# Performance work log

Measured on AMD Instinct MI355X. Metric: run time of the kernel, lower is better.

The kernel has to match this reference:

```python
import jax, jax.numpy as jnp
import numpy as np

NUM_HEADS = 16
HIDDEN = 1024
HEAD_DIM = HIDDEN // NUM_HEADS
B, S, D = 2, 2048, 1024


def setup_inputs() -> dict:
    key = jax.random.key(0)
    ks = jax.random.split(key, 7)
    scale = 1.0 / np.sqrt(D)
    return {
        "query": jax.random.normal(ks[0], (B, S, D), dtype=jnp.float32),
        "key": jax.random.normal(ks[1], (B, S, D), dtype=jnp.float32),
        "value": jax.random.normal(ks[2], (B, S, D), dtype=jnp.float32),
        "Wk_w": jax.random.normal(ks[3], (HIDDEN, D), dtype=jnp.float32) * scale,
        "Wk_b": jax.random.normal(ks[4], (HIDDEN,), dtype=jnp.float32) * scale,
        "Wv_w": jax.random.normal(ks[5], (HIDDEN, D), dtype=jnp.float32) * scale,
        "Wv_b": jax.random.normal(ks[6], (HIDDEN,), dtype=jnp.float32) * scale,
    }


def reference(query, key, value, Wk_w, Wk_b, Wv_w, Wv_b):
    # NOTE: in the original torch module, self.W_v is assigned twice, so the
    # SAME Linear (Wv) projects both key and value; Wk projects query.
    b, s, _ = query.shape

    def split_heads(x):  # [b,s,hidden] -> [b,h,s,hd]
        return x.reshape(b, s, NUM_HEADS, HEAD_DIM).transpose(0, 2, 1, 3)

    q = split_heads(query @ Wk_w.T + Wk_b)
    k = split_heads(key @ Wv_w.T + Wv_b)
    v = split_heads(value @ Wv_w.T + Wv_b)

    scores = jnp.einsum("bhqd,bhkd->bhqk", q, k) / jnp.sqrt(
        jnp.asarray(HEAD_DIM, dtype=q.dtype))
    probs = jax.nn.softmax(scores, axis=-1)
    out = jnp.einsum("bhqk,bhkd->bhqd", probs, v)
    return out.transpose(0, 2, 1, 3).reshape(b, s, NUM_HEADS * HEAD_DIM)
```

## Files before the change

### kernel.cpp

```cpp
#include <hip/hip_runtime.h>
#include <stdint.h>

typedef unsigned short u16;
typedef uint32_t u32;
typedef __bf16 bf16x8 __attribute__((ext_vector_type(8)));
typedef float f32x4 __attribute__((ext_vector_type(4)));
typedef float f32x16 __attribute__((ext_vector_type(16)));
typedef u16 u16x4 __attribute__((ext_vector_type(4)));
typedef u16 u16x8 __attribute__((ext_vector_type(8)));

#define XQ_OFF 0ul
#define XK_OFF 4194304ul
#define XV_OFF 8388608ul
#define WK_OFF 12582912ul
#define WV_OFF 13631488ul
#define Q_OFF  14680064ul
#define K_OFF  18874368ul
#define V_OFF  23068672ul

#define SCQ 0.18033688011112042f

#if __has_builtin(__builtin_amdgcn_exp2f)
#define EXP2F(x) __builtin_amdgcn_exp2f(x)
#else
#define EXP2F(x) exp2f(x)
#endif

__device__ __forceinline__ u16 f2bf(float f) {
  u32 u = __float_as_uint(f);
  u32 r = (u + 0x7fffu + ((u >> 16) & 1u)) >> 16;
  return (u16)r;
}

__device__ __forceinline__ u32 pk2(float a, float b) {
  typedef __bf16 bf2_t __attribute__((ext_vector_type(2)));
  typedef float f2_t __attribute__((ext_vector_type(2)));
  f2_t v; v[0] = a; v[1] = b;
  bf2_t h = __builtin_convertvector(v, bf2_t);
  union { bf2_t h; u32 u; } cv; cv.h = h; return cv.u;
}

__device__ __forceinline__ void load_lds16(const void* g, void* l) {
  __builtin_amdgcn_global_load_lds(
      (const __attribute__((address_space(1))) u32*)g,
      (__attribute__((address_space(3))) u32*)l, 16, 0, 0);
}

__global__ __launch_bounds__(256) void cvt_tile_kernel(
    const float* __restrict__ xq, const float* __restrict__ xk,
    const float* __restrict__ xv, const float* __restrict__ wk,
    const float* __restrict__ wv, u16* __restrict__ ws) {
  __shared__ u16 tile[4096];
  const int bid = blockIdx.x;
  const float* src; size_t dstbase; int rt, ktp;
  if (bid < 3072) {
    int m = bid >> 10, loc = bid & 1023;
    src = (m == 0) ? xq : (m == 1) ? xk : xv;
    dstbase = (size_t)m * 4194304ul;
    rt = loc >> 4; ktp = loc & 15;
  } else {
    int r2 = bid - 3072;
    int m = r2 >> 8, loc = r2 & 255;
    src = m ? wv : wk;
    dstbase = WK_OFF + (size_t)m * 1048576ul;
    rt = loc >> 4; ktp = loc & 15;
  }
  const int t = threadIdx.x;
  const int row0 = t >> 4, c = t & 15;
  const int k = c * 4;
  const float* s = src + (size_t)(rt * 64 + row0) * 1024ul + ktp * 64 + k;
#pragma unroll
  for (int i = 0; i < 4; ++i) {
    float4 v = *(const float4*)(s + (size_t)i * 16384ul);
    int row = row0 + i * 16;
    u32* p = (u32*)(tile + ((k >> 5) * 2048 + ((k >> 3) & 3) * 512 + row * 8 + (k & 7)));
    p[0] = pk2(v.x, v.y);
    p[1] = pk2(v.z, v.w);
  }
  __syncthreads();
  u16* dst = ws + dstbase + (size_t)(rt * 32 + ktp * 2) * 2048ul;
#pragma unroll
  for (int so = 0; so < 4096; so += 2048)
    *(u16x8*)(dst + so + t * 8) = *(const u16x8*)(tile + so + t * 8);
}

__global__ __launch_bounds__(256, 3) void proj_kernel(u16* __restrict__ ws,
                                                      const float* __restrict__ bk,
                                                      const float* __restrict__ bv) {
  const int proj = blockIdx.z;
  const int mtile = blockIdx.x;
  const int ntile = blockIdx.y;
  const u16* A = ws + (size_t)proj * 4194304ul;
  const u16* Bw = ws + ((proj == 0) ? WK_OFF : WV_OFF);
  const float* bias = (proj == 0) ? bk : bv;
  u16* outQ = ws + Q_OFF;
  u16* outK = ws + K_OFF;
  u16* outV = ws + V_OFF;

  const int t = threadIdx.x;
  const int w = t >> 6, lane = t & 63;
  const int wm = w >> 1, wn = w & 1;
  const int c32 = lane & 31, g2 = lane >> 5;

  const u16* Aw = A + (size_t)(2 * mtile + wm) * 65536ul + (size_t)g2 * 512ul + (size_t)c32 * 8ul;
  const u16* Bb = Bw + (size_t)(2 * ntile + wn) * 65536ul + (size_t)g2 * 512ul + (size_t)c32 * 8ul;

  f32x16 acc[2][2];
#pragma unroll
  for (int rf = 0; rf < 2; ++rf)
#pragma unroll
    for (int cf = 0; cf < 2; ++cf)
#pragma unroll
      for (int i = 0; i < 16; ++i) acc[rf][cf][i] = 0.f;

  bf16x8 ab[4][2], bb[4][2];
#pragma unroll
  for (int s = 0; s < 4; ++s)
#pragma unroll
    for (int f = 0; f < 2; ++f) {
      ab[s][f] = *(const bf16x8*)(Aw + (size_t)s * 1024ul + f * 256);
      bb[s][f] = *(const bf16x8*)(Bb + (size_t)s * 1024ul + f * 256);
    }

#pragma unroll 1
  for (int ks = 0; ks < 60; ks += 4) {
#pragma unroll
    for (int s = 0; s < 4; ++s) {
#pragma unroll
      for (int rf = 0; rf < 2; ++rf)
#pragma unroll
        for (int cf = 0; cf < 2; ++cf)
          acc[rf][cf] =
              __builtin_amdgcn_mfma_f32_32x32x16_bf16(ab[s][rf], bb[s][cf], acc[rf][cf], 0, 0, 0);
      const size_t o = (size_t)(ks + 4 + s) * 1024ul;
#pragma unroll
      for (int f = 0; f < 2; ++f) {
        ab[s][f] = *(const bf16x8*)(Aw + o + f * 256);
        bb[s][f] = *(const bf16x8*)(Bb + o + f * 256);
      }
    }
  }
#pragma unroll
  for (int s = 0; s < 4; ++s)
#pragma unroll
    for (int rf = 0; rf < 2; ++rf)
#pragma unroll
      for (int cf = 0; cf < 2; ++cf)
        acc[rf][cf] =
            __builtin_amdgcn_mfma_f32_32x32x16_bf16(ab[s][rf], bb[s][cf], acc[rf][cf], 0, 0, 0);

  const int m0w = mtile * 128 + wm * 64, n0w = ntile * 128 + wn * 64;
#pragma unroll
  for (int cf = 0; cf < 2; ++cf) {
    const int col = n0w + cf * 32 + c32;
    const float bvv = bias[col];
    const int h = col >> 6, d = col & 63;
#pragma unroll
    for (int rf = 0; rf < 2; ++rf) {
#pragma unroll
      for (int q = 0; q < 4; ++q) {
        const int mbase = m0w + rf * 32 + q * 8 + g2 * 4;
        const int b = mbase >> 11;
        const int bh = b * 16 + h;
        if (proj == 2) {
          const int s = mbase & 2047;
          u16x4 pk;
#pragma unroll
          for (int r = 0; r < 4; ++r) pk[r] = f2bf(acc[rf][cf][q * 4 + r] + bvv);
          size_t idx = (size_t)bh * 131072ul + (size_t)(s >> 6) * 4096ul +
                       (size_t)((s & 63) >> 3) * 512ul + (size_t)d * 8ul + (size_t)(s & 7);
          *(u16x4*)(outV + idx) = pk;
        } else {
          u16* dst = (proj == 0) ? outQ : outK;
#pragma unroll
          for (int r = 0; r < 4; ++r) {
            const int m = mbase + r;
            const int s = m & 2047;
            float y = acc[rf][cf][q * 4 + r] + bvv;
            if (proj == 0) y *= SCQ;
            size_t idx;
            if (proj == 0)
              idx = (size_t)bh * 131072ul + (size_t)(s >> 7) * 8192ul + (size_t)(d >> 3) * 1024ul +
                    (size_t)(s & 127) * 8ul + (size_t)(d & 7);
            else
              idx = (size_t)bh * 131072ul + (size_t)(s >> 6) * 4096ul + (size_t)(d >> 3) * 512ul +
                    (size_t)(s & 63) * 8ul + (size_t)(d & 7);
            dst[idx] = f2bf(y);
          }
        }
      }
    }
  }
}

__global__ __launch_bounds__(256, 2) void attn_kernel(const u16* __restrict__ ws,
                                                      float* __restrict__ out) {
  const int bh = blockIdx.x, qtile = blockIdx.y;
  const int b = bh >> 4, h = bh & 15;
  const int t = threadIdx.x, w = t >> 6, lane = t & 63, g = lane >> 4, c = lane & 15;

  __shared__ __align__(16) u16 Ps[4][1280];

  const u16* Qg = ws + Q_OFF + (size_t)bh * 131072ul + (size_t)qtile * 8192ul;
  const u16* Kg = ws + K_OFF + (size_t)bh * 131072ul;
  const u16* Vg = ws + V_OFF + (size_t)bh * 131072ul;

  bf16x8 qf[2][2];
#pragma unroll
  for (int ntq = 0; ntq < 2; ++ntq)
#pragma unroll
    for (int ks = 0; ks < 2; ++ks)
      qf[ntq][ks] = *(const bf16x8*)(Qg + (ks * 4 + g) * 1024 + (w * 32 + ntq * 16 + c) * 8);

  u16x8 ou;
#pragma unroll
  for (int i = 0; i < 8; ++i) ou[i] = (u16)0x3F80;
  union { u16x8 u; bf16x8 b; } ocv; ocv.u = ou;
  const bf16x8 onesf = ocv.b;

  f32x4 O[2][4], Lacc[2];
#pragma unroll
  for (int mtq = 0; mtq < 2; ++mtq) {
    Lacc[mtq] = (f32x4){0.f, 0.f, 0.f, 0.f};
#pragma unroll
    for (int nt = 0; nt < 4; ++nt) O[mtq][nt] = (f32x4){0.f, 0.f, 0.f, 0.f};
  }

  u16* Psw = Ps[w];

  bf16x8 kf[2][4];
#pragma unroll
  for (int ks = 0; ks < 2; ++ks)
#pragma unroll
    for (int mtk = 0; mtk < 4; ++mtk)
      kf[ks][mtk] = *(const bf16x8*)(Kg + (ks * 4 + g) * 512 + (mtk * 16 + c) * 8);

#pragma unroll 1
  for (int j = 0; j < 32; ++j) {
    const u16* Vj = Vg + (size_t)j * 4096ul;
    bf16x8 vf[2][4];
#pragma unroll
    for (int ksh = 0; ksh < 2; ++ksh)
#pragma unroll
      for (int nt = 0; nt < 4; ++nt)
        vf[ksh][nt] = *(const bf16x8*)(Vj + (ksh * 4 + g) * 512 + (nt * 16 + c) * 8);

    f32x4 St[4][2];
#pragma unroll
    for (int mtk = 0; mtk < 4; ++mtk)
#pragma unroll
      for (int ntq = 0; ntq < 2; ++ntq) St[mtk][ntq] = (f32x4){0.f, 0.f, 0.f, 0.f};
#pragma unroll
    for (int ks = 0; ks < 2; ++ks)
#pragma unroll
      for (int mtk = 0; mtk < 4; ++mtk)
#pragma unroll
        for (int ntq = 0; ntq < 2; ++ntq)
          St[mtk][ntq] =
              __builtin_amdgcn_mfma_f32_16x16x32_bf16(kf[ks][mtk], qf[ntq][ks], St[mtk][ntq], 0, 0, 0);

    const u16* Kn = Kg + (size_t)((j < 31) ? (j + 1) : 31) * 4096ul;
#pragma unroll
    for (int ks = 0; ks < 2; ++ks)
#pragma unroll
      for (int mtk = 0; mtk < 4; ++mtk)
        kf[ks][mtk] = *(const bf16x8*)(Kn + (ks * 4 + g) * 512 + (mtk * 16 + c) * 8);

#pragma unroll
    for (int mtk = 0; mtk < 4; ++mtk)
#pragma unroll
      for (int ntq = 0; ntq < 2; ++ntq)
#pragma unroll
        for (int r = 0; r < 4; ++r) St[mtk][ntq][r] = EXP2F(St[mtk][ntq][r]);

#pragma unroll
    for (int ksh = 0; ksh < 2; ++ksh) {
#pragma unroll
      for (int ntq = 0; ntq < 2; ++ntq)
#pragma unroll
        for (int m2 = 0; m2 < 2; ++m2) {
          const int mtk = ksh * 2 + m2;
          u32 lo = pk2(St[mtk][ntq][0], St[mtk][ntq][1]);
          u32 hi = pk2(St[mtk][ntq][2], St[mtk][ntq][3]);
          u32* p = (u32*)(Psw + (ntq * 16 + c) * 40 + m2 * 16 + g * 4);
          p[0] = lo; p[1] = hi;
        }
      asm volatile("s_waitcnt lgkmcnt(0)" ::: "memory");
      bf16x8 pf[2];
#pragma unroll
      for (int mtq = 0; mtq < 2; ++mtq)
        pf[mtq] = *(const bf16x8*)(Psw + (mtq * 16 + c) * 40 + g * 8);
#pragma unroll
      for (int mtq = 0; mtq < 2; ++mtq) {
        Lacc[mtq] = __builtin_amdgcn_mfma_f32_16x16x32_bf16(pf[mtq], onesf, Lacc[mtq], 0, 0, 0);
#pragma unroll
        for (int nt = 0; nt < 4; ++nt)
          O[mtq][nt] =
              __builtin_amdgcn_mfma_f32_16x16x32_bf16(pf[mtq], vf[ksh][nt], O[mtq][nt], 0, 0, 0);
      }
    }
  }

  const int q0 = qtile * 128 + w * 32;
#pragma unroll
  for (int mtq = 0; mtq < 2; ++mtq)
#pragma unroll
    for (int r = 0; r < 4; ++r) {
      const float inv = 1.0f / Lacc[mtq][r];
      const int q = q0 + mtq * 16 + g * 4 + r;
      float* rowp = out + (size_t)(b * 2048 + q) * 1024ul + h * 64;
#pragma unroll
      for (int nt = 0; nt < 4; ++nt) rowp[nt * 16 + c] = O[mtq][nt][r] * inv;
    }
}

extern "C" void kernel_launch(void* const* d_in, const int* in_sizes, int n_in,
                              void* d_out, int out_size, void* d_ws, size_t ws_size,
                              hipStream_t stream) {
  const float* q = (const float*)d_in[0];
  const float* k = (const float*)d_in[1];
  const float* v = (const float*)d_in[2];
  const float* wk = (const float*)d_in[3];
  const float* bk = (const float*)d_in[4];
  const float* wv = (const float*)d_in[5];
  const float* bv = (const float*)d_in[6];
  u16* ws = (u16*)d_ws;
  float* out = (float*)d_out;

  cvt_tile_kernel<<<3584, 256, 0, stream>>>(q, k, v, wk, wv, ws);
  proj_kernel<<<dim3(32, 8, 3), 256, 0, stream>>>(ws, bk, bv);
  attn_kernel<<<dim3(32, 16), 256, 0, stream>>>(ws, out);
}
```

Before: 180.0 us.

## Stage projection and K/V tiles through swizzled double-buffered LDS

The projection GEMM now loads A and B tiles into double-buffered LDS with direct global-to-LDS copies and an XOR swizzle, computing with 16x16x32 MFMAs instead of per-wave register streaming from global memory. The attention kernel likewise shares each K/V block across all four waves through double-buffered swizzled LDS rather than each wave reading its own copy. It also halves the query rows per block and doubles the grid, with higher occupancy bounds. This is meant to cut redundant global/L2 traffic and raise parallelism, at the cost of a block-wide barrier every iteration and more LDS use.

```diff
diff --git a/kernel.cpp b/kernel.cpp
--- a/kernel.cpp
+++ b/kernel.cpp
@@ -5,7 +5,6 @@
 typedef uint32_t u32;
 typedef __bf16 bf16x8 __attribute__((ext_vector_type(8)));
 typedef float f32x4 __attribute__((ext_vector_type(4)));
-typedef float f32x16 __attribute__((ext_vector_type(16)));
 typedef u16 u16x4 __attribute__((ext_vector_type(4)));
 typedef u16 u16x8 __attribute__((ext_vector_type(8)));
 
@@ -44,6 +43,10 @@
   __builtin_amdgcn_global_load_lds(
       (const __attribute__((address_space(1))) u32*)g,
       (__attribute__((address_space(3))) u32*)l, 16, 0, 0);
+}
+
+__device__ __forceinline__ u32 swz(u32 L) {
+  return L ^ (((L >> 7) & 1u) << 4) ^ (((L >> 10) & 3u) << 5);
 }
 
 __global__ __launch_bounds__(256) void cvt_tile_kernel(
@@ -100,117 +103,131 @@
   const int t = threadIdx.x;
   const int w = t >> 6, lane = t & 63;
   const int wm = w >> 1, wn = w & 1;
-  const int c32 = lane & 31, g2 = lane >> 5;
-
-  const u16* Aw = A + (size_t)(2 * mtile + wm) * 65536ul + (size_t)g2 * 512ul + (size_t)c32 * 8ul;
-  const u16* Bb = Bw + (size_t)(2 * ntile + wn) * 65536ul + (size_t)g2 * 512ul + (size_t)c32 * 8ul;
-
-  f32x16 acc[2][2];
-#pragma unroll
-  for (int rf = 0; rf < 2; ++rf)
-#pragma unroll
-    for (int cf = 0; cf < 2; ++cf)
-#pragma unroll
-      for (int i = 0; i < 16; ++i) acc[rf][cf][i] = 0.f;
-
-  bf16x8 ab[4][2], bb[4][2];
-#pragma unroll
-  for (int s = 0; s < 4; ++s)
-#pragma unroll
-    for (int f = 0; f < 2; ++f) {
-      ab[s][f] = *(const bf16x8*)(Aw + (size_t)s * 1024ul + f * 256);
-      bb[s][f] = *(const bf16x8*)(Bb + (size_t)s * 1024ul + f * 256);
-    }
+  const int g = lane >> 4, c = lane & 15;
+
+  __shared__ __align__(16) u16 As[2][2][2048];
+  __shared__ __align__(16) u16 Bs[2][2][2048];
+
+  const u16* Ag = A + (size_t)(2 * mtile) * 65536ul;
+  const u16* Bg = Bw + (size_t)(2 * ntile) * 65536ul;
+  const u32 t8 = (u32)t * 8u;
+  const u32 so = swz((u32)t * 16u) >> 1;
+
+  u32 poff[4];
+#pragma unroll
+  for (int mt = 0; mt < 4; ++mt)
+    poff[mt] = swz((u32)((g << 10) | ((mt * 16 + c) << 4))) >> 1;
+
+#define PSTAGE(buf, kt)                                            \
+  do {                                                             \
+    const size_t ko = (size_t)(kt) * 2048ul + so;                  \
+    load_lds16(Ag + ko, &As[buf][0][t8]);                          \
+    load_lds16(Ag + 65536ul + ko, &As[buf][1][t8]);                \
+    load_lds16(Bg + ko, &Bs[buf][0][t8]);                          \
+    load_lds16(Bg + 65536ul + ko, &Bs[buf][1][t8]);                \
+  } while (0)
+
+  f32x4 acc[4][4];
+#pragma unroll
+  for (int mt = 0; mt < 4; ++mt)
+#pragma unroll
+    for (int nt = 0; nt < 4; ++nt) acc[mt][nt] = (f32x4){0.f, 0.f, 0.f, 0.f};
+
+  PSTAGE(0, 0);
+  __syncthreads();
 
 #pragma unroll 1
-  for (int ks = 0; ks < 60; ks += 4) {
-#pragma unroll
-    for (int s = 0; s < 4; ++s) {
-#pragma unroll
-      for (int rf = 0; rf < 2; ++rf)
-#pragma unroll
-        for (int cf = 0; cf < 2; ++cf)
-          acc[rf][cf] =
-              __builtin_amdgcn_mfma_f32_32x32x16_bf16(ab[s][rf], bb[s][cf], acc[rf][cf], 0, 0, 0);
-      const size_t o = (size_t)(ks + 4 + s) * 1024ul;
-#pragma unroll
-      for (int f = 0; f < 2; ++f) {
-        ab[s][f] = *(const bf16x8*)(Aw + o + f * 256);
-        bb[s][f] = *(const bf16x8*)(Bb + o + f * 256);
-      }
-    }
-  }
-#pragma unroll
-  for (int s = 0; s < 4; ++s)
-#pragma unroll
-    for (int rf = 0; rf < 2; ++rf)
-#pragma unroll
-      for (int cf = 0; cf < 2; ++cf)
-        acc[rf][cf] =
-            __builtin_amdgcn_mfma_f32_32x32x16_bf16(ab[s][rf], bb[s][cf], acc[rf][cf], 0, 0, 0);
-
-  const int m0w = mtile * 128 + wm * 64, n0w = ntile * 128 + wn * 64;
-#pragma unroll
-  for (int cf = 0; cf < 2; ++cf) {
-    const int col = n0w + cf * 32 + c32;
+  for (int kt = 0; kt < 32; ++kt) {
+    const int cur = kt & 1;
+    if (kt < 31) PSTAGE(cur ^ 1, kt + 1);
+    const u16* Ap = As[cur][wm];
+    const u16* Bp = Bs[cur][wn];
+    bf16x8 af[4], bf[4];
+#pragma unroll
+    for (int mt = 0; mt < 4; ++mt) af[mt] = *(const bf16x8*)(Ap + poff[mt]);
+#pragma unroll
+    for (int nt = 0; nt < 4; ++nt) bf[nt] = *(const bf16x8*)(Bp + poff[nt]);
+#pragma unroll
+    for (int mt = 0; mt < 4; ++mt)
+#pragma unroll
+      for (int nt = 0; nt < 4; ++nt)
+        acc[mt][nt] =
+            __builtin_amdgcn_mfma_f32_16x16x32_bf16(af[mt], bf[nt], acc[mt][nt], 0, 0, 0);
+    __syncthreads();
+  }
+#undef PSTAGE
+
+  const int m0 = mtile * 128 + wm * 64;
+  const int n0 = ntile * 128 + wn * 64;
+#pragma unroll
+  for (int nt = 0; nt < 4; ++nt) {
+    const int col = n0 + nt * 16 + c;
     const float bvv = bias[col];
     const int h = col >> 6, d = col & 63;
 #pragma unroll
-    for (int rf = 0; rf < 2; ++rf) {
-#pragma unroll
-      for (int q = 0; q < 4; ++q) {
-        const int mbase = m0w + rf * 32 + q * 8 + g2 * 4;
-        const int b = mbase >> 11;
-        const int bh = b * 16 + h;
-        if (proj == 2) {
-          const int s = mbase & 2047;
-          u16x4 pk;
-#pragma unroll
-          for (int r = 0; r < 4; ++r) pk[r] = f2bf(acc[rf][cf][q * 4 + r] + bvv);
-          size_t idx = (size_t)bh * 131072ul + (size_t)(s >> 6) * 4096ul +
-                       (size_t)((s & 63) >> 3) * 512ul + (size_t)d * 8ul + (size_t)(s & 7);
-          *(u16x4*)(outV + idx) = pk;
-        } else {
-          u16* dst = (proj == 0) ? outQ : outK;
-#pragma unroll
-          for (int r = 0; r < 4; ++r) {
-            const int m = mbase + r;
-            const int s = m & 2047;
-            float y = acc[rf][cf][q * 4 + r] + bvv;
-            if (proj == 0) y *= SCQ;
-            size_t idx;
-            if (proj == 0)
-              idx = (size_t)bh * 131072ul + (size_t)(s >> 7) * 8192ul + (size_t)(d >> 3) * 1024ul +
-                    (size_t)(s & 127) * 8ul + (size_t)(d & 7);
-            else
-              idx = (size_t)bh * 131072ul + (size_t)(s >> 6) * 4096ul + (size_t)(d >> 3) * 512ul +
-                    (size_t)(s & 63) * 8ul + (size_t)(d & 7);
-            dst[idx] = f2bf(y);
-          }
+    for (int mt = 0; mt < 4; ++mt) {
+      const int mbase = m0 + mt * 16 + g * 4;
+      const int b = mbase >> 11;
+      const int bh = b * 16 + h;
+      const int s = mbase & 2047;
+      if (proj == 2) {
+        u16x4 pk;
+#pragma unroll
+        for (int r = 0; r < 4; ++r) pk[r] = f2bf(acc[mt][nt][r] + bvv);
+        size_t idx = (size_t)bh * 131072ul + (size_t)(s >> 6) * 4096ul +
+                     (size_t)((s & 63) >> 3) * 512ul + (size_t)d * 8ul + (size_t)(s & 7);
+        *(u16x4*)(outV + idx) = pk;
+      } else {
+        u16* dst = (proj == 0) ? outQ : outK;
+#pragma unroll
+        for (int r = 0; r < 4; ++r) {
+          const int m = mbase + r;
+          const int s2 = m & 2047;
+          float y = acc[mt][nt][r] + bvv;
+          if (proj == 0) y *= SCQ;
+          size_t idx;
+          if (proj == 0)
+            idx = (size_t)bh * 131072ul + (size_t)(s2 >> 7) * 8192ul + (size_t)(d >> 3) * 1024ul +
+                  (size_t)(s2 & 127) * 8ul + (size_t)(d & 7);
+          else
+            idx = (size_t)bh * 131072ul + (size_t)(s2 >> 6) * 4096ul + (size_t)(d >> 3) * 512ul +
+                  (size_t)(s2 & 63) * 8ul + (size_t)(d & 7);
+          dst[idx] = f2bf(y);
         }
       }
     }
   }
 }
 
-__global__ __launch_bounds__(256, 2) void attn_kernel(const u16* __restrict__ ws,
+__global__ __launch_bounds__(256, 4) void attn_kernel(const u16* __restrict__ ws,
                                                       float* __restrict__ out) {
-  const int bh = blockIdx.x, qtile = blockIdx.y;
+  const int bh = blockIdx.x, qb = blockIdx.y;
   const int b = bh >> 4, h = bh & 15;
   const int t = threadIdx.x, w = t >> 6, lane = t & 63, g = lane >> 4, c = lane & 15;
 
-  __shared__ __align__(16) u16 Ps[4][1280];
-
-  const u16* Qg = ws + Q_OFF + (size_t)bh * 131072ul + (size_t)qtile * 8192ul;
+  __shared__ __align__(16) u16 Ks[2][4096];
+  __shared__ __align__(16) u16 Vs[2][4096];
+  __shared__ __align__(16) u16 Ps[4][640];
+
+  const u16* Qg = ws + Q_OFF + (size_t)bh * 131072ul + (size_t)(qb >> 1) * 8192ul;
   const u16* Kg = ws + K_OFF + (size_t)bh * 131072ul;
   const u16* Vg = ws + V_OFF + (size_t)bh * 131072ul;
 
-  bf16x8 qf[2][2];
-#pragma unroll
-  for (int ntq = 0; ntq < 2; ++ntq)
-#pragma unroll
-    for (int ks = 0; ks < 2; ++ks)
-      qf[ntq][ks] = *(const bf16x8*)(Qg + (ks * 4 + g) * 1024 + (w * 32 + ntq * 16 + c) * 8);
+  const u32 t8 = (u32)t * 8u;
+  const u32 so0 = swz((u32)t * 16u) >> 1;
+  const u32 so1 = swz(4096u + (u32)t * 16u) >> 1;
+  u32 off[2][4];
+#pragma unroll
+  for (int a = 0; a < 2; ++a)
+#pragma unroll
+    for (int mA = 0; mA < 4; ++mA)
+      off[a][mA] = swz((u32)(((a * 4 + g) << 10) | ((mA * 16 + c) << 4))) >> 1;
+
+  const int qrow = (qb & 1) * 64 + w * 16 + c;
+  bf16x8 qf[2];
+#pragma unroll
+  for (int ks = 0; ks < 2; ++ks)
+    qf[ks] = *(const bf16x8*)(Qg + (size_t)(ks * 4 + g) * 1024ul + (size_t)qrow * 8ul);
 
   u16x8 ou;
 #pragma unroll
@@ -218,100 +235,84 @@
   union { u16x8 u; bf16x8 b; } ocv; ocv.u = ou;
   const bf16x8 onesf = ocv.b;
 
-  f32x4 O[2][4], Lacc[2];
-#pragma unroll
-  for (int mtq = 0; mtq < 2; ++mtq) {
-    Lacc[mtq] = (f32x4){0.f, 0.f, 0.f, 0.f};
-#pragma unroll
-    for (int nt = 0; nt < 4; ++nt) O[mtq][nt] = (f32x4){0.f, 0.f, 0.f, 0.f};
-  }
+  f32x4 O[4], Lacc;
+  Lacc = (f32x4){0.f, 0.f, 0.f, 0.f};
+#pragma unroll
+  for (int nt = 0; nt < 4; ++nt) O[nt] = (f32x4){0.f, 0.f, 0.f, 0.f};
 
   u16* Psw = Ps[w];
 
-  bf16x8 kf[2][4];
-#pragma unroll
-  for (int ks = 0; ks < 2; ++ks)
-#pragma unroll
-    for (int mtk = 0; mtk < 4; ++mtk)
-      kf[ks][mtk] = *(const bf16x8*)(Kg + (ks * 4 + g) * 512 + (mtk * 16 + c) * 8);
+#define STAGE_KV(buf, jj)                                       \
+  do {                                                          \
+    const u16* Kj = Kg + (size_t)(jj) * 4096ul;                 \
+    const u16* Vj = Vg + (size_t)(jj) * 4096ul;                 \
+    load_lds16(Kj + so0, &Ks[buf][t8]);                         \
+    load_lds16(Kj + so1, &Ks[buf][t8 + 2048]);                  \
+    load_lds16(Vj + so0, &Vs[buf][t8]);                         \
+    load_lds16(Vj + so1, &Vs[buf][t8 + 2048]);                  \
+  } while (0)
+
+  STAGE_KV(0, 0);
+  __syncthreads();
 
 #pragma unroll 1
   for (int j = 0; j < 32; ++j) {
-    const u16* Vj = Vg + (size_t)j * 4096ul;
-    bf16x8 vf[2][4];
-#pragma unroll
-    for (int ksh = 0; ksh < 2; ++ksh)
+    const int cur = j & 1;
+    if (j < 31) STAGE_KV(cur ^ 1, j + 1);
+    const u16* Kb = Ks[cur];
+    const u16* Vb = Vs[cur];
+
+    f32x4 St[4];
+#pragma unroll
+    for (int mtk = 0; mtk < 4; ++mtk) St[mtk] = (f32x4){0.f, 0.f, 0.f, 0.f};
+#pragma unroll
+    for (int ks = 0; ks < 2; ++ks) {
+      bf16x8 kfv[4];
+#pragma unroll
+      for (int mtk = 0; mtk < 4; ++mtk) kfv[mtk] = *(const bf16x8*)(Kb + off[ks][mtk]);
+#pragma unroll
+      for (int mtk = 0; mtk < 4; ++mtk)
+        St[mtk] = __builtin_amdgcn_mfma_f32_16x16x32_bf16(kfv[mtk], qf[ks], St[mtk], 0, 0, 0);
+    }
+
+#pragma unroll
+    for (int mtk = 0; mtk < 4; ++mtk)
+#pragma unroll
+      for (int r = 0; r < 4; ++r) St[mtk][r] = EXP2F(St[mtk][r]);
+
+#pragma unroll
+    for (int ksh = 0; ksh < 2; ++ksh) {
+#pragma unroll
+      for (int m2 = 0; m2 < 2; ++m2) {
+        const int mtk = ksh * 2 + m2;
+        u32 lo = pk2(St[mtk][0], St[mtk][1]);
+        u32 hi = pk2(St[mtk][2], St[mtk][3]);
+        u32* p = (u32*)(Psw + c * 40 + m2 * 16 + g * 4);
+        p[0] = lo; p[1] = hi;
+      }
+      bf16x8 vfv[4];
+#pragma unroll
+      for (int nt = 0; nt < 4; ++nt) vfv[nt] = *(const bf16x8*)(Vb + off[ksh][nt]);
+      asm volatile("s_waitcnt lgkmcnt(0)" ::: "memory");
+      bf16x8 pf = *(const bf16x8*)(Psw + c * 40 + g * 8);
+      Lacc = __builtin_amdgcn_mfma_f32_16x16x32_bf16(pf, onesf, Lacc, 0, 0, 0);
 #pragma unroll
       for (int nt = 0; nt < 4; ++nt)
-        vf[ksh][nt] = *(const bf16x8*)(Vj + (ksh * 4 + g) * 512 + (nt * 16 + c) * 8);
-
-    f32x4 St[4][2];
-#pragma unroll
-    for (int mtk = 0; mtk < 4; ++mtk)
-#pragma unroll
-      for (int ntq = 0; ntq < 2; ++ntq) St[mtk][ntq] = (f32x4){0.f, 0.f, 0.f, 0.f};
-#pragma unroll
-    for (int ks = 0; ks < 2; ++ks)
-#pragma unroll
-      for (int mtk = 0; mtk < 4; ++mtk)
-#pragma unroll
-        for (int ntq = 0; ntq < 2; ++ntq)
-          St[mtk][ntq] =
-              __builtin_amdgcn_mfma_f32_16x16x32_bf16(kf[ks][mtk], qf[ntq][ks], St[mtk][ntq], 0, 0, 0);
-
-    const u16* Kn = Kg + (size_t)((j < 31) ? (j + 1) : 31) * 4096ul;
-#pragma unroll
-    for (int ks = 0; ks < 2; ++ks)
-#pragma unroll
-      for (int mtk = 0; mtk < 4; ++mtk)
-        kf[ks][mtk] = *(const bf16x8*)(Kn + (ks * 4 + g) * 512 + (mtk * 16 + c) * 8);
-
-#pragma unroll
-    for (int mtk = 0; mtk < 4; ++mtk)
-#pragma unroll
-      for (int ntq = 0; ntq < 2; ++ntq)
-#pragma unroll
-        for (int r = 0; r < 4; ++r) St[mtk][ntq][r] = EXP2F(St[mtk][ntq][r]);
-
-#pragma unroll
-    for (int ksh = 0; ksh < 2; ++ksh) {
-#pragma unroll
-      for (int ntq = 0; ntq < 2; ++ntq)
-#pragma unroll
-        for (int m2 = 0; m2 < 2; ++m2) {
-          const int mtk = ksh * 2 + m2;
-          u32 lo = pk2(St[mtk][ntq][0], St[mtk][ntq][1]);
-          u32 hi = pk2(St[mtk][ntq][2], St[mtk][ntq][3]);
-          u32* p = (u32*)(Psw + (ntq * 16 + c) * 40 + m2 * 16 + g * 4);
-          p[0] = lo; p[1] = hi;
-        }
-      asm volatile("s_waitcnt lgkmcnt(0)" ::: "memory");
-      bf16x8 pf[2];
-#pragma unroll
-      for (int mtq = 0; mtq < 2; ++mtq)
-        pf[mtq] = *(const bf16x8*)(Psw + (mtq * 16 + c) * 40 + g * 8);
-#pragma unroll
-      for (int mtq = 0; mtq < 2; ++mtq) {
-        Lacc[mtq] = __builtin_amdgcn_mfma_f32_16x16x32_bf16(pf[mtq], onesf, Lacc[mtq], 0, 0, 0);
-#pragma unroll
-        for (int nt = 0; nt < 4; ++nt)
-          O[mtq][nt] =
-              __builtin_amdgcn_mfma_f32_16x16x32_bf16(pf[mtq], vf[ksh][nt], O[mtq][nt], 0, 0, 0);
-      }
+        O[nt] = __builtin_amdgcn_mfma_f32_16x16x32_bf16(pf, vfv[nt], O[nt], 0, 0, 0);
     }
-  }
-
-  const int q0 = qtile * 128 + w * 32;
-#pragma unroll
-  for (int mtq = 0; mtq < 2; ++mtq)
-#pragma unroll
-    for (int r = 0; r < 4; ++r) {
-      const float inv = 1.0f / Lacc[mtq][r];
-      const int q = q0 + mtq * 16 + g * 4 + r;
-      float* rowp = out + (size_t)(b * 2048 + q) * 1024ul + h * 64;
-#pragma unroll
-      for (int nt = 0; nt < 4; ++nt) rowp[nt * 16 + c] = O[mtq][nt][r] * inv;
-    }
+    __syncthreads();
+  }
+#undef STAGE_KV
+
+  const int q0 = qb * 64 + w * 16;
+#pragma unroll
+  for (int r = 0; r < 4; ++r) {
+    const float inv = 1.0f / Lacc[r];
+    const int q = q0 + g * 4 + r;
+    float* rowp = out + (size_t)(b * 2048 + q) * 1024ul + h * 64;
+#pragma unroll
+    for (int nt = 0; nt < 4; ++nt) rowp[nt * 16 + c] = O[nt][r] * inv;
+  }
 }
 
 extern "C" void kernel_launch(void* const* d_in, const int* in_sizes, int n_in,
@@ -329,5 +330,5 @@
 
   cvt_tile_kernel<<<3584, 256, 0, stream>>>(q, k, v, wk, wv, ws);
   proj_kernel<<<dim3(32, 8, 3), 256, 0, stream>>>(ws, bk, bv);
-  attn_kernel<<<dim3(32, 16), 256, 0, stream>>>(ws, out);
-}
+  attn_kernel<<<dim3(32, 32), 256, 0, stream>>>(ws, out);
+}
```

New measurement: 192.3 us. +6.9%, slower.
